# Kernel tuning notes

Measured on AMD Instinct MI355X. Metric: run time of the kernel, lower is better.

The kernel has to match this reference:

```python
import jax, jax.numpy as jnp
import numpy as np

N_NODES = 100000

def _sage_conv(x, src, dst, W_l, b_l, W_r):
    # PyG SAGEConv (aggr='mean'): out = lin_l(mean_{j in N(i)} x_j) + lin_r(x_i)
    msg = x[src]                                             # [E, d] gather
    agg = jax.ops.segment_sum(msg, dst, num_segments=N_NODES)  # [N, d]
    deg = jax.ops.segment_sum(jnp.ones((src.shape[0],), x.dtype), dst,
                              num_segments=N_NODES)          # [N]
    mean = agg / jnp.maximum(deg, 1.0)[:, None]
    return mean @ W_l + b_l + x @ W_r

def setup_inputs() -> dict:
    key = jax.random.key(0)
    ks = jax.random.split(key, 8)
    d_in, d_hid, d_out = 128, 128, 64
    E = 1_600_000
    x = jax.random.normal(ks[0], (N_NODES, d_in), dtype=jnp.float32)
    edge_index = jax.random.randint(ks[1], (2, E), 0, N_NODES, dtype=jnp.int64)
    s1 = 1.0 / np.sqrt(d_in)
    s2 = 1.0 / np.sqrt(d_hid)
    return {
        "x": x,
        "W1_l": jax.random.uniform(ks[2], (d_in, d_hid), jnp.float32, -s1, s1),
        "b1":   jnp.zeros((d_hid,), jnp.float32),
        "W1_r": jax.random.uniform(ks[3], (d_in, d_hid), jnp.float32, -s1, s1),
        "W2_l": jax.random.uniform(ks[4], (d_hid, d_out), jnp.float32, -s2, s2),
        "b2":   jnp.zeros((d_out,), jnp.float32),
        "W2_r": jax.random.uniform(ks[5], (d_hid, d_out), jnp.float32, -s2, s2),
        "edge_index": edge_index,
    }

def reference(x, W1_l, b1, W1_r, W2_l, b2, W2_r, edge_index):
    src, dst = edge_index[0], edge_index[1]
    h = _sage_conv(x, src, dst, W1_l, b1, W1_r)
    h = jax.nn.relu(h)
    # dropout is identity in eval mode (p=0.5 train-only); omitted for determinism
    out = _sage_conv(h, src, dst, W2_l, b2, W2_r)
    return out
```

## Files before the change

### kernel.cpp

```cpp
#include <hip/hip_runtime.h>
#include <hip/hip_bf16.h>
#include <cstdint>


typedef __bf16 bf16x8 __attribute__((ext_vector_type(8)));
typedef float f32x4 __attribute__((ext_vector_type(4)));
typedef float f32x2 __attribute__((ext_vector_type(2)));

#define MAXBUCK 800
#define CAP 2560
#define MAXEPT 16
#define P2B 512
#define HSTRIDE 136

__device__ __forceinline__ unsigned short f2bf(float f) {
    union { float f; unsigned int u; } v; v.f = f;
    unsigned int u = v.u;
    unsigned int r = ((u >> 16) & 1u) + 0x7fffu;
    return (unsigned short)((u + r) >> 16);
}

__device__ __forceinline__ f32x2 up2(unsigned int u) {
    uint2 t; t.x = u << 16; t.y = u & 0xffff0000u;
    return __builtin_bit_cast(f32x2, t);
}
__device__ __forceinline__ void accp(const uint4& v, f32x2* a) {
    a[0] += up2(v.x);
    a[1] += up2(v.y);
    a[2] += up2(v.z);
    a[3] += up2(v.w);
}
__device__ __forceinline__ void accpw(const uint4& v, float w, f32x2* a) {
    a[0] += up2(v.x) * w;
    a[1] += up2(v.y) * w;
    a[2] += up2(v.z) * w;
    a[3] += up2(v.w) * w;
}

__device__ __forceinline__ int edge_val(const int* ei32, const long long* ei64,
                                        int is64, size_t idx) {
    return is64 ? (int)ei64[idx] : ei32[idx];
}

__global__ __launch_bounds__(256) void fused_front(const float* __restrict__ x,
                                                   unsigned short* __restrict__ xb,
                                                   long long n8, int ncvt,
                                                   const float* __restrict__ W1l,
                                                   const float* __restrict__ W1r,
                                                   uint4* __restrict__ w1frag,
                                                   const float* __restrict__ W2l,
                                                   const float* __restrict__ W2r,
                                                   uint4* __restrict__ w2frag,
                                                   const int* __restrict__ ei32,
                                                   const long long* __restrict__ ei64,
                                                   int E, int ept, int nbuck,
                                                   int n_nodes,
                                                   int* __restrict__ bucket_pos,
                                                   unsigned* __restrict__ ebuf) {
    __shared__ int lhist[MAXBUCK];
    __shared__ int gbase[MAXBUCK];
    int b = blockIdx.x;
    if (b < P2B) {
        for (int i = threadIdx.x; i < nbuck; i += 256) lhist[i] = 0;
        __syncthreads();
        int is64;
        {
            int ok = 1;
            for (int i = 0; i < 8; ++i) {
                long long v = ei64[i];
                if (v < 0 || v >= n_nodes) ok = 0;
            }
            is64 = ok;
        }
        int base_e = b * (ept * 256);
        unsigned ed[MAXEPT];
        int bidx[MAXEPT];
        int slot[MAXEPT];
#pragma unroll 4
        for (int i = 0; i < ept; ++i) {
            int e = base_e + i * 256 + threadIdx.x;
            if (e < E) {
                int s = edge_val(ei32, ei64, is64, (size_t)e);
                int d = edge_val(ei32, ei64, is64, (size_t)E + e);
                ed[i] = ((unsigned)s << 7) | (unsigned)(d & 127);
                bidx[i] = d >> 7;
                slot[i] = atomicAdd(&lhist[d >> 7], 1);
            } else {
                slot[i] = -1;
            }
        }
        __syncthreads();
        for (int i = threadIdx.x; i < nbuck; i += 256) {
            int c = lhist[i];
            gbase[i] = c ? atomicAdd(&bucket_pos[i], c) : 0;
        }
        __syncthreads();
#pragma unroll 4
        for (int i = 0; i < ept; ++i) {
            if (slot[i] >= 0) {
                int pos = gbase[bidx[i]] + slot[i];
                if (pos < CAP) ebuf[(size_t)bidx[i] * CAP + pos] = ed[i];
            }
        }
        return;
    }
    int cb = b - P2B;
    if (cb < ncvt) {
        long long i = (long long)cb * 256 + threadIdx.x;
        if (i >= n8) return;
        const float4* p = (const float4*)(x + i * 8);
        float4 a = p[0], c = p[1];
        uint4 o;
        o.x = (unsigned)f2bf(a.x) | ((unsigned)f2bf(a.y) << 16);
        o.y = (unsigned)f2bf(a.z) | ((unsigned)f2bf(a.w) << 16);
        o.z = (unsigned)f2bf(c.x) | ((unsigned)f2bf(c.y) << 16);
        o.w = (unsigned)f2bf(c.z) | ((unsigned)f2bf(c.w) << 16);
        ((uint4*)(xb))[i] = o;
        return;
    }
    if (cb < ncvt + 16) {
        int tid = (cb - ncvt) * 256 + threadIdx.x;
        int fi = tid >> 6, lane = tid & 63;
        int ct = fi >> 3, ks = fi & 7;
        int k0 = ks * 32 + (lane >> 4) * 8;
        int n = ct * 16 + (lane & 15);
        unsigned short e[8];
#pragma unroll
        for (int j = 0; j < 8; ++j) {
            int k = k0 + j;
            float v = (k < 128) ? W1l[k * 128 + n] : W1r[(k - 128) * 128 + n];
            e[j] = f2bf(v);
        }
        uint4 o;
        o.x = (unsigned)e[0] | ((unsigned)e[1] << 16);
        o.y = (unsigned)e[2] | ((unsigned)e[3] << 16);
        o.z = (unsigned)e[4] | ((unsigned)e[5] << 16);
        o.w = (unsigned)e[6] | ((unsigned)e[7] << 16);
        w1frag[tid] = o;
        return;
    }
    int tid = (cb - ncvt - 16) * 256 + threadIdx.x;
    if (tid >= 2048) return;
    int fi = tid >> 6, lane = tid & 63;
    int ct = fi >> 2, ks = fi & 3;
    int k0 = ks * 32 + (lane >> 4) * 8;
    int n = ct * 16 + (lane & 15);
    unsigned short e[8];
#pragma unroll
    for (int j = 0; j < 8; ++j) {
        int k = k0 + j;
        float v = (n < 64) ? W2l[k * 64 + n] : W2r[k * 64 + (n - 64)];
        e[j] = f2bf(v);
    }
    uint4 o;
    o.x = (unsigned)e[0] | ((unsigned)e[1] << 16);
    o.y = (unsigned)e[2] | ((unsigned)e[3] << 16);
    o.z = (unsigned)e[4] | ((unsigned)e[5] << 16);
    o.w = (unsigned)e[6] | ((unsigned)e[7] << 16);
    w2frag[tid] = o;
}

__global__ __launch_bounds__(256) void pass3_finalize(const unsigned* __restrict__ ebuf,
                                                      const int* __restrict__ bucket_pos,
                                                      int nbuck, int N,
                                                      int2* __restrict__ startcnt,
                                                      int* __restrict__ csr) {
    __shared__ int lcnt[128];
    __shared__ int lexcl[128];
    __shared__ int sc[128];
    int b = blockIdx.x;
    int t = threadIdx.x;
    int d0 = b << 7;
    int nb = N - d0; if (nb > 128) nb = 128;
    int m = bucket_pos[b]; if (m > CAP) m = CAP;
    const unsigned* eb = ebuf + (size_t)b * CAP;

    if (t < 128) lcnt[t] = 0;
    __syncthreads();
    for (int j = t; j < m; j += 256) {
        atomicAdd(&lcnt[eb[j] & 127u], 1);
    }
    __syncthreads();
    int v = 0;
    if (t < 128) { v = lcnt[t]; sc[t] = v; }
    __syncthreads();
    for (int o = 1; o < 128; o <<= 1) {
        int x = 0;
        if (t < 128 && t >= o) x = sc[t - o];
        __syncthreads();
        if (t < 128 && t >= o) sc[t] += x;
        __syncthreads();
    }
    if (t < 128) {
        int excl = sc[t] - v;
        lexcl[t] = excl;
        if (t < nb) startcnt[d0 + t] = make_int2(b * CAP + excl, v);
        lcnt[t] = 0;
    }
    __syncthreads();
    for (int j = t; j < m; j += 256) {
        unsigned ed = eb[j];
        int li = (int)(ed & 127u);
        int slot = atomicAdd(&lcnt[li], 1);
        csr[b * CAP + lexcl[li] + slot] = (int)(ed >> 7);
    }
}

__global__ __launch_bounds__(256) void agg_mean128_bf(const unsigned short* __restrict__ Xb,
                                                      const int2* __restrict__ startcnt,
                                                      const int* __restrict__ csr,
                                                      unsigned short* __restrict__ outb,
                                                      int n_nodes) {
    int node = blockIdx.x * 4 + (threadIdx.x >> 6);
    if (node >= n_nodes) return;
    int lane = threadIdx.x & 63;
    int quad = lane >> 4;
    int l16 = lane & 15;
    int2 sc2 = startcnt[node];
    int s0 = sc2.x, deg = sc2.y, s1 = s0 + deg;
    f32x2 A0[4], A1[4];
#pragma unroll
    for (int k = 0; k < 4; ++k) { A0[k] = (f32x2){0.f, 0.f}; A1[k] = (f32x2){0.f, 0.f}; }
    int j = s0;
    for (; j + 8 <= s1; j += 8) {
        int p0 = csr[j + quad];
        int p1 = csr[j + 4 + quad];
        uint4 v0 = ((const uint4*)(Xb + (size_t)p0 * 128))[l16];
        uint4 v1 = ((const uint4*)(Xb + (size_t)p1 * 128))[l16];
        accp(v0, A0);
        accp(v1, A1);
    }
    if (j + 4 <= s1) {
        int p = csr[j + quad];
        uint4 v = ((const uint4*)(Xb + (size_t)p * 128))[l16];
        accp(v, A0);
        j += 4;
    }
    if (j < s1) {
        int jj = j + quad;
        int p = csr[(jj < s1) ? jj : (s1 - 1)];
        float w = (jj < s1) ? 1.0f : 0.0f;
        uint4 v = ((const uint4*)(Xb + (size_t)p * 128))[l16];
        accpw(v, w, A1);
    }
    float r[8];
#pragma unroll
    for (int k = 0; k < 4; ++k) {
        f32x2 s = A0[k] + A1[k];
        r[2 * k] = s.x;
        r[2 * k + 1] = s.y;
    }
#pragma unroll
    for (int k = 0; k < 8; ++k) r[k] += __shfl(r[k], lane ^ 16);
#pragma unroll
    for (int k = 0; k < 8; ++k) r[k] += __shfl(r[k], lane ^ 32);
    float inv = (deg > 0) ? 1.0f / (float)deg : 0.0f;
    if (quad == 0) {
        uint4 o;
        o.x = (unsigned)f2bf(r[0] * inv) | ((unsigned)f2bf(r[1] * inv) << 16);
        o.y = (unsigned)f2bf(r[2] * inv) | ((unsigned)f2bf(r[3] * inv) << 16);
        o.z = (unsigned)f2bf(r[4] * inv) | ((unsigned)f2bf(r[5] * inv) << 16);
        o.w = (unsigned)f2bf(r[6] * inv) | ((unsigned)f2bf(r[7] * inv) << 16);
        ((uint4*)(outb + (size_t)node * 128))[l16] = o;
    }
}

__global__ __launch_bounds__(256) void agg_mean64_bf_ep(const unsigned short* __restrict__ Zb,
                                                        const float* __restrict__ Wadd,
                                                        const int2* __restrict__ startcnt,
                                                        const int* __restrict__ csr,
                                                        float* __restrict__ out,
                                                        int n_nodes) {
    int node = blockIdx.x * 4 + (threadIdx.x >> 6);
    if (node >= n_nodes) return;
    int lane = threadIdx.x & 63;
    int oct = lane >> 3;
    int l8 = lane & 7;
    int2 sc2 = startcnt[node];
    int s0 = sc2.x, deg = sc2.y, s1 = s0 + deg;
    f32x2 A0[4], A1[4];
#pragma unroll
    for (int k = 0; k < 4; ++k) { A0[k] = (f32x2){0.f, 0.f}; A1[k] = (f32x2){0.f, 0.f}; }
    int j = s0;
    for (; j + 16 <= s1; j += 16) {
        int p0 = csr[j + oct];
        int p1 = csr[j + 8 + oct];
        uint4 v0 = ((const uint4*)(Zb + (size_t)p0 * 64))[l8];
        uint4 v1 = ((const uint4*)(Zb + (size_t)p1 * 64))[l8];
        accp(v0, A0);
        accp(v1, A1);
    }
    if (j + 8 <= s1) {
        int p = csr[j + oct];
        uint4 v = ((const uint4*)(Zb + (size_t)p * 64))[l8];
        accp(v, A0);
        j += 8;
    }
    if (j < s1) {
        int jj = j + oct;
        int p = csr[(jj < s1) ? jj : (s1 - 1)];
        float w = (jj < s1) ? 1.0f : 0.0f;
        uint4 v = ((const uint4*)(Zb + (size_t)p * 64))[l8];
        accpw(v, w, A1);
    }
    float r[8];
#pragma unroll
    for (int k = 0; k < 4; ++k) {
        f32x2 s = A0[k] + A1[k];
        r[2 * k] = s.x;
        r[2 * k + 1] = s.y;
    }
#pragma unroll
    for (int k = 0; k < 8; ++k) r[k] += __shfl(r[k], lane ^ 8);
#pragma unroll
    for (int k = 0; k < 8; ++k) r[k] += __shfl(r[k], lane ^ 16);
#pragma unroll
    for (int k = 0; k < 8; ++k) r[k] += __shfl(r[k], lane ^ 32);
    float inv = (deg > 0) ? 1.0f / (float)deg : 0.0f;
    if (oct == 0) {
        const float4* wp = (const float4*)(Wadd + (size_t)node * 64 + l8 * 8);
        float4 w0 = wp[0], w1 = wp[1];
        float4 o0, o1;
        o0.x = r[0] * inv + w0.x; o0.y = r[1] * inv + w0.y;
        o0.z = r[2] * inv + w0.z; o0.w = r[3] * inv + w0.w;
        o1.x = r[4] * inv + w1.x; o1.y = r[5] * inv + w1.y;
        o1.z = r[6] * inv + w1.z; o1.w = r[7] * inv + w1.w;
        float4* op = (float4*)(out + (size_t)node * 64 + l8 * 8);
        op[0] = o0; op[1] = o1;
    }
}

__global__ __launch_bounds__(256, 3) void gemm12_mfma(const unsigned short* __restrict__ meanb,
                                                      const unsigned short* __restrict__ xb,
                                                      const uint4* __restrict__ w1frag,
                                                      const uint4* __restrict__ w2frag,
                                                      const float* __restrict__ b1,
                                                      const float* __restrict__ b2,
                                                      unsigned short* __restrict__ z2,
                                                      float* __restrict__ w2out,
                                                      int nrows) {
    __shared__ unsigned short hs[4][32 * HSTRIDE];
    const int wid = threadIdx.x >> 6, lane = threadIdx.x & 63;
    const int quad = lane >> 4, l16 = lane & 15;
    const int m0 = blockIdx.x * 128 + wid * 32;
    unsigned short* hsw = &hs[wid][0];
    const uint4* w1p = w1frag + lane;
    const uint4* w2p = w2frag + lane;

    bf16x8 af[2][8];
#pragma unroll
    for (int mt = 0; mt < 2; ++mt) {
        int row = m0 + mt * 16 + l16;
        int rowc = (row < nrows) ? row : (nrows - 1);
        const uint4* mrow = (const uint4*)(meanb + (size_t)rowc * 128);
        const uint4* xrow = (const uint4*)(xb + (size_t)rowc * 128);
#pragma unroll
        for (int ks = 0; ks < 4; ++ks) {
            af[mt][ks]     = __builtin_bit_cast(bf16x8, mrow[ks * 4 + quad]);
            af[mt][ks + 4] = __builtin_bit_cast(bf16x8, xrow[ks * 4 + quad]);
        }
    }

    uint4 wc[8], wn[8];
#pragma unroll
    for (int ks = 0; ks < 8; ++ks) wc[ks] = w1p[ks * 64];
#pragma unroll
    for (int ct = 0; ct < 8; ++ct) {
        if (ct < 7) {
#pragma unroll
            for (int ks = 0; ks < 8; ++ks) wn[ks] = w1p[((ct + 1) * 8 + ks) * 64];
        }
        f32x4 a0 = (f32x4){0.f, 0.f, 0.f, 0.f};
        f32x4 a1 = (f32x4){0.f, 0.f, 0.f, 0.f};
#pragma unroll
        for (int ks = 0; ks < 8; ++ks) {
            bf16x8 bf = __builtin_bit_cast(bf16x8, wc[ks]);
            a0 = __builtin_amdgcn_mfma_f32_16x16x32_bf16(af[0][ks], bf, a0, 0, 0, 0);
            a1 = __builtin_amdgcn_mfma_f32_16x16x32_bf16(af[1][ks], bf, a1, 0, 0, 0);
        }
        int col = ct * 16 + l16;
        float bb = b1[col];
#pragma unroll
        for (int r = 0; r < 4; ++r) {
            hsw[(quad * 4 + r) * HSTRIDE + col] = f2bf(fmaxf(a0[r] + bb, 0.f));
            hsw[(16 + quad * 4 + r) * HSTRIDE + col] = f2bf(fmaxf(a1[r] + bb, 0.f));
        }
#pragma unroll
        for (int ks = 0; ks < 8; ++ks) wc[ks] = wn[ks];
    }

    bf16x8 af2[2][4];
#pragma unroll
    for (int mt = 0; mt < 2; ++mt)
#pragma unroll
        for (int ks = 0; ks < 4; ++ks) {
            uint4 t = *(const uint4*)(hsw + (mt * 16 + l16) * HSTRIDE + ks * 32 + quad * 8);
            af2[mt][ks] = __builtin_bit_cast(bf16x8, t);
        }

    uint4 wc2[4], wn2[4];
#pragma unroll
    for (int ks = 0; ks < 4; ++ks) wc2[ks] = w2p[ks * 64];
#pragma unroll
    for (int ct = 0; ct < 8; ++ct) {
        if (ct < 7) {
#pragma unroll
            for (int ks = 0; ks < 4; ++ks) wn2[ks] = w2p[((ct + 1) * 4 + ks) * 64];
        }
        f32x4 a0 = (f32x4){0.f, 0.f, 0.f, 0.f};
        f32x4 a1 = (f32x4){0.f, 0.f, 0.f, 0.f};
#pragma unroll
        for (int ks = 0; ks < 4; ++ks) {
            bf16x8 bf = __builtin_bit_cast(bf16x8, wc2[ks]);
            a0 = __builtin_amdgcn_mfma_f32_16x16x32_bf16(af2[0][ks], bf, a0, 0, 0, 0);
            a1 = __builtin_amdgcn_mfma_f32_16x16x32_bf16(af2[1][ks], bf, a1, 0, 0, 0);
        }
        int col = ct * 16 + l16;
#pragma unroll
        for (int mt = 0; mt < 2; ++mt) {
            f32x4 acc = mt ? a1 : a0;
#pragma unroll
            for (int r = 0; r < 4; ++r) {
                int orow = m0 + mt * 16 + quad * 4 + r;
                if (orow < nrows) {
                    if (col < 64) {
                        z2[(size_t)orow * 64 + col] = f2bf(acc[r]);
                    } else {
                        w2out[(size_t)orow * 64 + (col - 64)] = acc[r] + b2[col - 64];
                    }
                }
            }
        }
#pragma unroll
        for (int ks = 0; ks < 4; ++ks) wc2[ks] = wn2[ks];
    }
}

extern "C" void kernel_launch(void* const* d_in, const int* in_sizes, int n_in,
                              void* d_out, int out_size, void* d_ws, size_t ws_size,
                              hipStream_t stream) {
    const float* x    = (const float*)d_in[0];
    const float* W1_l = (const float*)d_in[1];
    const float* b1   = (const float*)d_in[2];
    const float* W1_r = (const float*)d_in[3];
    const float* W2_l = (const float*)d_in[4];
    const float* b2   = (const float*)d_in[5];
    const float* W2_r = (const float*)d_in[6];
    const void*  ei   = d_in[7];
    float* out = (float*)d_out;

    const int N = in_sizes[0] / 128;
    const int E = in_sizes[7] / 2;
    const int nbuck = (N + 127) >> 7;

    uintptr_t base = (uintptr_t)d_ws;
    int* bucket_pos = (int*)(base + 64);
    int2* startcnt = (int2*)(base + 8192);
    int* csr = (int*)((uintptr_t)(startcnt + N) + 255 & ~(uintptr_t)255);
    uintptr_t p = ((uintptr_t)(csr + (size_t)nbuck * CAP) + 255) & ~(uintptr_t)255;
    unsigned short* xb    = (unsigned short*)p; p += (size_t)N * 128 * 2;
    unsigned short* meanb = (unsigned short*)p; p += (size_t)N * 128 * 2;
    unsigned short* hbr   = (unsigned short*)p; p += (size_t)N * 128 * 2;
    uint4* w1frag = (uint4*)p; p += 4096 * 16;
    uint4* w2frag = (uint4*)p; p += 2048 * 16;
    unsigned* ebuf = (unsigned*)meanb;
    unsigned short* z2 = hbr;
    float* w2 = (float*)xb;

    const int* ei32 = (const int*)ei;
    const long long* ei64 = (const long long*)ei;

    hipMemsetAsync(bucket_pos, 0, (size_t)nbuck * sizeof(int), stream);

    long long n8 = (long long)N * 128 / 8;
    int ncvt = (int)((n8 + 255) / 256);
    int ept = (E + P2B * 256 - 1) / (P2B * 256);

    fused_front<<<P2B + ncvt + 24, 256, 0, stream>>>(
        x, xb, n8, ncvt, W1_l, W1_r, w1frag, W2_l, W2_r, w2frag,
        ei32, ei64, E, ept, nbuck, N, bucket_pos, ebuf);

    pass3_finalize<<<nbuck, 256, 0, stream>>>(ebuf, bucket_pos, nbuck, N,
                                              startcnt, csr);

    int ablocks = (N + 3) / 4;
    int gblocks = (N + 127) / 128;

    agg_mean128_bf<<<ablocks, 256, 0, stream>>>(xb, startcnt, csr, meanb, N);
    gemm12_mfma<<<gblocks, 256, 0, stream>>>(meanb, xb, w1frag, w2frag, b1, b2,
                                             z2, w2, N);
    agg_mean64_bf_ep<<<ablocks, 256, 0, stream>>>(z2, w2, startcnt, csr, out, N);
}
```

Baseline: 272.0 us.

## Fuse CSR finalize, layer-1 mean aggregation and both GEMMs into one kernel

Merges the bucket finalize, 128-wide mean aggregation and the fused layer-1/layer-2 MFMA GEMM into a single per-bucket kernel. The CSR slice is kept in LDS and the aggregated means are written straight into the per-wave LDS tile the GEMM reads, so the meanb round trip through global memory and two launches go away. In exchange, each 256-thread block now handles 128 nodes serially (32 per wave), so only about 782 blocks run, parallelism for the gather phase drops sharply, and LDS use per block grows. The workspace layout is also reorganised because ebuf and xb can no longer alias.

```diff
diff --git a/kernel.cpp b/kernel.cpp
--- a/kernel.cpp
+++ b/kernel.cpp
@@ -160,17 +160,27 @@
     w2frag[tid] = o;
 }
 
-__global__ __launch_bounds__(256) void pass3_finalize(const unsigned* __restrict__ ebuf,
-                                                      const int* __restrict__ bucket_pos,
-                                                      int nbuck, int N,
-                                                      int2* __restrict__ startcnt,
-                                                      int* __restrict__ csr) {
+__global__ __launch_bounds__(256, 3) void fused_mid(const unsigned* __restrict__ ebuf,
+                                                    const int* __restrict__ bucket_pos,
+                                                    const unsigned short* __restrict__ xb,
+                                                    const uint4* __restrict__ w1frag,
+                                                    const uint4* __restrict__ w2frag,
+                                                    const float* __restrict__ b1,
+                                                    const float* __restrict__ b2,
+                                                    int2* __restrict__ startcnt,
+                                                    int* __restrict__ csr,
+                                                    unsigned short* __restrict__ z2,
+                                                    float* __restrict__ w2out,
+                                                    int N) {
     __shared__ int lcnt[128];
     __shared__ int lexcl[128];
     __shared__ int sc[128];
-    int b = blockIdx.x;
-    int t = threadIdx.x;
-    int d0 = b << 7;
+    __shared__ int csr_s[CAP];
+    __shared__ unsigned short hs[4][32 * HSTRIDE];
+
+    const int b = blockIdx.x;
+    const int t = threadIdx.x;
+    const int d0 = b << 7;
     int nb = N - d0; if (nb > 128) nb = 128;
     int m = bucket_pos[b]; if (m > CAP) m = CAP;
     const unsigned* eb = ebuf + (size_t)b * CAP;
@@ -185,10 +195,10 @@
     if (t < 128) { v = lcnt[t]; sc[t] = v; }
     __syncthreads();
     for (int o = 1; o < 128; o <<= 1) {
-        int x = 0;
-        if (t < 128 && t >= o) x = sc[t - o];
+        int xx = 0;
+        if (t < 128 && t >= o) xx = sc[t - o];
         __syncthreads();
-        if (t < 128 && t >= o) sc[t] += x;
+        if (t < 128 && t >= o) sc[t] += xx;
         __syncthreads();
     }
     if (t < 128) {
@@ -202,66 +212,158 @@
         unsigned ed = eb[j];
         int li = (int)(ed & 127u);
         int slot = atomicAdd(&lcnt[li], 1);
-        csr[b * CAP + lexcl[li] + slot] = (int)(ed >> 7);
-    }
-}
-
-__global__ __launch_bounds__(256) void agg_mean128_bf(const unsigned short* __restrict__ Xb,
-                                                      const int2* __restrict__ startcnt,
-                                                      const int* __restrict__ csr,
-                                                      unsigned short* __restrict__ outb,
-                                                      int n_nodes) {
-    int node = blockIdx.x * 4 + (threadIdx.x >> 6);
-    if (node >= n_nodes) return;
-    int lane = threadIdx.x & 63;
-    int quad = lane >> 4;
-    int l16 = lane & 15;
-    int2 sc2 = startcnt[node];
-    int s0 = sc2.x, deg = sc2.y, s1 = s0 + deg;
-    f32x2 A0[4], A1[4];
-#pragma unroll
-    for (int k = 0; k < 4; ++k) { A0[k] = (f32x2){0.f, 0.f}; A1[k] = (f32x2){0.f, 0.f}; }
-    int j = s0;
-    for (; j + 8 <= s1; j += 8) {
-        int p0 = csr[j + quad];
-        int p1 = csr[j + 4 + quad];
-        uint4 v0 = ((const uint4*)(Xb + (size_t)p0 * 128))[l16];
-        uint4 v1 = ((const uint4*)(Xb + (size_t)p1 * 128))[l16];
-        accp(v0, A0);
-        accp(v1, A1);
-    }
-    if (j + 4 <= s1) {
-        int p = csr[j + quad];
-        uint4 v = ((const uint4*)(Xb + (size_t)p * 128))[l16];
-        accp(v, A0);
-        j += 4;
-    }
-    if (j < s1) {
-        int jj = j + quad;
-        int p = csr[(jj < s1) ? jj : (s1 - 1)];
-        float w = (jj < s1) ? 1.0f : 0.0f;
-        uint4 v = ((const uint4*)(Xb + (size_t)p * 128))[l16];
-        accpw(v, w, A1);
-    }
-    float r[8];
-#pragma unroll
-    for (int k = 0; k < 4; ++k) {
-        f32x2 s = A0[k] + A1[k];
-        r[2 * k] = s.x;
-        r[2 * k + 1] = s.y;
-    }
-#pragma unroll
-    for (int k = 0; k < 8; ++k) r[k] += __shfl(r[k], lane ^ 16);
-#pragma unroll
-    for (int k = 0; k < 8; ++k) r[k] += __shfl(r[k], lane ^ 32);
-    float inv = (deg > 0) ? 1.0f / (float)deg : 0.0f;
-    if (quad == 0) {
-        uint4 o;
-        o.x = (unsigned)f2bf(r[0] * inv) | ((unsigned)f2bf(r[1] * inv) << 16);
-        o.y = (unsigned)f2bf(r[2] * inv) | ((unsigned)f2bf(r[3] * inv) << 16);
-        o.z = (unsigned)f2bf(r[4] * inv) | ((unsigned)f2bf(r[5] * inv) << 16);
-        o.w = (unsigned)f2bf(r[6] * inv) | ((unsigned)f2bf(r[7] * inv) << 16);
-        ((uint4*)(outb + (size_t)node * 128))[l16] = o;
+        int pos = lexcl[li] + slot;
+        int sv = (int)(ed >> 7);
+        csr_s[pos] = sv;
+        csr[b * CAP + pos] = sv;
+    }
+    __syncthreads();
+
+    const int wid = t >> 6, lane = t & 63;
+    const int quad = lane >> 4, l16 = lane & 15;
+    unsigned short* hsw = &hs[wid][0];
+    for (int ln = 0; ln < 32; ++ln) {
+        int li = wid * 32 + ln;
+        int deg = lcnt[li];
+        int s0l = lexcl[li];
+        f32x2 A0[4], A1[4];
+#pragma unroll
+        for (int k = 0; k < 4; ++k) { A0[k] = (f32x2){0.f, 0.f}; A1[k] = (f32x2){0.f, 0.f}; }
+        int j = 0;
+        for (; j + 8 <= deg; j += 8) {
+            int p0 = csr_s[s0l + j + quad];
+            int p1 = csr_s[s0l + j + 4 + quad];
+            uint4 v0 = ((const uint4*)(xb + (size_t)p0 * 128))[l16];
+            uint4 v1 = ((const uint4*)(xb + (size_t)p1 * 128))[l16];
+            accp(v0, A0);
+            accp(v1, A1);
+        }
+        if (j + 4 <= deg) {
+            int p = csr_s[s0l + j + quad];
+            uint4 v0 = ((const uint4*)(xb + (size_t)p * 128))[l16];
+            accp(v0, A0);
+            j += 4;
+        }
+        if (j < deg) {
+            int jj = j + quad;
+            int p = csr_s[s0l + ((jj < deg) ? jj : (deg - 1))];
+            float w = (jj < deg) ? 1.0f : 0.0f;
+            uint4 v0 = ((const uint4*)(xb + (size_t)p * 128))[l16];
+            accpw(v0, w, A1);
+        }
+        float r[8];
+#pragma unroll
+        for (int k = 0; k < 4; ++k) {
+            f32x2 s = A0[k] + A1[k];
+            r[2 * k] = s.x;
+            r[2 * k + 1] = s.y;
+        }
+#pragma unroll
+        for (int k = 0; k < 8; ++k) r[k] += __shfl(r[k], lane ^ 16);
+#pragma unroll
+        for (int k = 0; k < 8; ++k) r[k] += __shfl(r[k], lane ^ 32);
+        float inv = (deg > 0) ? 1.0f / (float)deg : 0.0f;
+        if (quad == 0) {
+            uint4 o;
+            o.x = (unsigned)f2bf(r[0] * inv) | ((unsigned)f2bf(r[1] * inv) << 16);
+            o.y = (unsigned)f2bf(r[2] * inv) | ((unsigned)f2bf(r[3] * inv) << 16);
+            o.z = (unsigned)f2bf(r[4] * inv) | ((unsigned)f2bf(r[5] * inv) << 16);
+            o.w = (unsigned)f2bf(r[6] * inv) | ((unsigned)f2bf(r[7] * inv) << 16);
+            *(uint4*)(hsw + ln * HSTRIDE + l16 * 8) = o;
+        }
+    }
+
+    const int m0 = d0 + wid * 32;
+    const uint4* w1p = w1frag + lane;
+    const uint4* w2p = w2frag + lane;
+
+    bf16x8 af[2][8];
+#pragma unroll
+    for (int mt = 0; mt < 2; ++mt) {
+        int rl = mt * 16 + l16;
+        int grow = m0 + rl;
+        int rowc = (grow < N) ? grow : (N - 1);
+        const uint4* xrow = (const uint4*)(xb + (size_t)rowc * 128);
+#pragma unroll
+        for (int ks = 0; ks < 4; ++ks) {
+            af[mt][ks]     = __builtin_bit_cast(bf16x8,
+                *(const uint4*)(hsw + rl * HSTRIDE + ks * 32 + quad * 8));
+            af[mt][ks + 4] = __builtin_bit_cast(bf16x8, xrow[ks * 4 + quad]);
+        }
+    }
+
+    uint4 wc[8], wn[8];
+#pragma unroll
+    for (int ks = 0; ks < 8; ++ks) wc[ks] = w1p[ks * 64];
+#pragma unroll
+    for (int ct = 0; ct < 8; ++ct) {
+        if (ct < 7) {
+#pragma unroll
+            for (int ks = 0; ks < 8; ++ks) wn[ks] = w1p[((ct + 1) * 8 + ks) * 64];
+        }
+        f32x4 a0 = (f32x4){0.f, 0.f, 0.f, 0.f};
+        f32x4 a1 = (f32x4){0.f, 0.f, 0.f, 0.f};
+#pragma unroll
+        for (int ks = 0; ks < 8; ++ks) {
+            bf16x8 bf = __builtin_bit_cast(bf16x8, wc[ks]);
+            a0 = __builtin_amdgcn_mfma_f32_16x16x32_bf16(af[0][ks], bf, a0, 0, 0, 0);
+            a1 = __builtin_amdgcn_mfma_f32_16x16x32_bf16(af[1][ks], bf, a1, 0, 0, 0);
+        }
+        int col = ct * 16 + l16;
+        float bb = b1[col];
+#pragma unroll
+        for (int r = 0; r < 4; ++r) {
+            hsw[(quad * 4 + r) * HSTRIDE + col] = f2bf(fmaxf(a0[r] + bb, 0.f));
+            hsw[(16 + quad * 4 + r) * HSTRIDE + col] = f2bf(fmaxf(a1[r] + bb, 0.f));
+        }
+#pragma unroll
+        for (int ks = 0; ks < 8; ++ks) wc[ks] = wn[ks];
+    }
+
+    bf16x8 af2[2][4];
+#pragma unroll
+    for (int mt = 0; mt < 2; ++mt)
+#pragma unroll
+        for (int ks = 0; ks < 4; ++ks) {
+            uint4 tt = *(const uint4*)(hsw + (mt * 16 + l16) * HSTRIDE + ks * 32 + quad * 8);
+            af2[mt][ks] = __builtin_bit_cast(bf16x8, tt);
+        }
+
+    uint4 wc2[4], wn2[4];
+#pragma unroll
+    for (int ks = 0; ks < 4; ++ks) wc2[ks] = w2p[ks * 64];
+#pragma unroll
+    for (int ct = 0; ct < 8; ++ct) {
+        if (ct < 7) {
+#pragma unroll
+            for (int ks = 0; ks < 4; ++ks) wn2[ks] = w2p[((ct + 1) * 4 + ks) * 64];
+        }
+        f32x4 a0 = (f32x4){0.f, 0.f, 0.f, 0.f};
+        f32x4 a1 = (f32x4){0.f, 0.f, 0.f, 0.f};
+#pragma unroll
+        for (int ks = 0; ks < 4; ++ks) {
+            bf16x8 bf = __builtin_bit_cast(bf16x8, wc2[ks]);
+            a0 = __builtin_amdgcn_mfma_f32_16x16x32_bf16(af2[0][ks], bf, a0, 0, 0, 0);
+            a1 = __builtin_amdgcn_mfma_f32_16x16x32_bf16(af2[1][ks], bf, a1, 0, 0, 0);
+        }
+        int col = ct * 16 + l16;
+#pragma unroll
+        for (int mt = 0; mt < 2; ++mt) {
+            f32x4 acc = mt ? a1 : a0;
+#pragma unroll
+            for (int r = 0; r < 4; ++r) {
+                int orow = m0 + mt * 16 + quad * 4 + r;
+                if (orow < N) {
+                    if (col < 64) {
+                        z2[(size_t)orow * 64 + col] = f2bf(acc[r]);
+                    } else {
+                        w2out[(size_t)orow * 64 + (col - 64)] = acc[r] + b2[col - 64];
+                    }
+                }
+            }
+        }
+#pragma unroll
+        for (int ks = 0; ks < 4; ++ks) wc2[ks] = wn2[ks];
     }
 }
 
@@ -330,112 +432,6 @@
     }
 }
 
-__global__ __launch_bounds__(256, 3) void gemm12_mfma(const unsigned short* __restrict__ meanb,
-                                                      const unsigned short* __restrict__ xb,
-                                                      const uint4* __restrict__ w1frag,
-                                                      const uint4* __restrict__ w2frag,
-                                                      const float* __restrict__ b1,
-                                                      const float* __restrict__ b2,
-                                                      unsigned short* __restrict__ z2,
-                                                      float* __restrict__ w2out,
-                                                      int nrows) {
-    __shared__ unsigned short hs[4][32 * HSTRIDE];
-    const int wid = threadIdx.x >> 6, lane = threadIdx.x & 63;
-    const int quad = lane >> 4, l16 = lane & 15;
-    const int m0 = blockIdx.x * 128 + wid * 32;
-    unsigned short* hsw = &hs[wid][0];
-    const uint4* w1p = w1frag + lane;
-    const uint4* w2p = w2frag + lane;
-
-    bf16x8 af[2][8];
-#pragma unroll
-    for (int mt = 0; mt < 2; ++mt) {
-        int row = m0 + mt * 16 + l16;
-        int rowc = (row < nrows) ? row : (nrows - 1);
-        const uint4* mrow = (const uint4*)(meanb + (size_t)rowc * 128);
-        const uint4* xrow = (const uint4*)(xb + (size_t)rowc * 128);
-#pragma unroll
-        for (int ks = 0; ks < 4; ++ks) {
-            af[mt][ks]     = __builtin_bit_cast(bf16x8, mrow[ks * 4 + quad]);
-            af[mt][ks + 4] = __builtin_bit_cast(bf16x8, xrow[ks * 4 + quad]);
-        }
-    }
-
-    uint4 wc[8], wn[8];
-#pragma unroll
-    for (int ks = 0; ks < 8; ++ks) wc[ks] = w1p[ks * 64];
-#pragma unroll
-    for (int ct = 0; ct < 8; ++ct) {
-        if (ct < 7) {
-#pragma unroll
-            for (int ks = 0; ks < 8; ++ks) wn[ks] = w1p[((ct + 1) * 8 + ks) * 64];
-        }
-        f32x4 a0 = (f32x4){0.f, 0.f, 0.f, 0.f};
-        f32x4 a1 = (f32x4){0.f, 0.f, 0.f, 0.f};
-#pragma unroll
-        for (int ks = 0; ks < 8; ++ks) {
-            bf16x8 bf = __builtin_bit_cast(bf16x8, wc[ks]);
-            a0 = __builtin_amdgcn_mfma_f32_16x16x32_bf16(af[0][ks], bf, a0, 0, 0, 0);
-            a1 = __builtin_amdgcn_mfma_f32_16x16x32_bf16(af[1][ks], bf, a1, 0, 0, 0);
-        }
-        int col = ct * 16 + l16;
-        float bb = b1[col];
-#pragma unroll
-        for (int r = 0; r < 4; ++r) {
-            hsw[(quad * 4 + r) * HSTRIDE + col] = f2bf(fmaxf(a0[r] + bb, 0.f));
-            hsw[(16 + quad * 4 + r) * HSTRIDE + col] = f2bf(fmaxf(a1[r] + bb, 0.f));
-        }
-#pragma unroll
-        for (int ks = 0; ks < 8; ++ks) wc[ks] = wn[ks];
-    }
-
-    bf16x8 af2[2][4];
-#pragma unroll
-    for (int mt = 0; mt < 2; ++mt)
-#pragma unroll
-        for (int ks = 0; ks < 4; ++ks) {
-            uint4 t = *(const uint4*)(hsw + (mt * 16 + l16) * HSTRIDE + ks * 32 + quad * 8);
-            af2[mt][ks] = __builtin_bit_cast(bf16x8, t);
-        }
-
-    uint4 wc2[4], wn2[4];
-#pragma unroll
-    for (int ks = 0; ks < 4; ++ks) wc2[ks] = w2p[ks * 64];
-#pragma unroll
-    for (int ct = 0; ct < 8; ++ct) {
-        if (ct < 7) {
-#pragma unroll
-            for (int ks = 0; ks < 4; ++ks) wn2[ks] = w2p[((ct + 1) * 4 + ks) * 64];
-        }
-        f32x4 a0 = (f32x4){0.f, 0.f, 0.f, 0.f};
-        f32x4 a1 = (f32x4){0.f, 0.f, 0.f, 0.f};
-#pragma unroll
-        for (int ks = 0; ks < 4; ++ks) {
-            bf16x8 bf = __builtin_bit_cast(bf16x8, wc2[ks]);
-            a0 = __builtin_amdgcn_mfma_f32_16x16x32_bf16(af2[0][ks], bf, a0, 0, 0, 0);
-            a1 = __builtin_amdgcn_mfma_f32_16x16x32_bf16(af2[1][ks], bf, a1, 0, 0, 0);
-        }
-        int col = ct * 16 + l16;
-#pragma unroll
-        for (int mt = 0; mt < 2; ++mt) {
-            f32x4 acc = mt ? a1 : a0;
-#pragma unroll
-            for (int r = 0; r < 4; ++r) {
-                int orow = m0 + mt * 16 + quad * 4 + r;
-                if (orow < nrows) {
-                    if (col < 64) {
-                        z2[(size_t)orow * 64 + col] = f2bf(acc[r]);
-                    } else {
-                        w2out[(size_t)orow * 64 + (col - 64)] = acc[r] + b2[col - 64];
-                    }
-                }
-            }
-        }
-#pragma unroll
-        for (int ks = 0; ks < 4; ++ks) wc2[ks] = wn2[ks];
-    }
-}
-
 extern "C" void kernel_launch(void* const* d_in, const int* in_sizes, int n_in,
                               void* d_out, int out_size, void* d_ws, size_t ws_size,
                               hipStream_t stream) {
@@ -456,16 +452,15 @@
     uintptr_t base = (uintptr_t)d_ws;
     int* bucket_pos = (int*)(base + 64);
     int2* startcnt = (int2*)(base + 8192);
-    int* csr = (int*)((uintptr_t)(startcnt + N) + 255 & ~(uintptr_t)255);
-    uintptr_t p = ((uintptr_t)(csr + (size_t)nbuck * CAP) + 255) & ~(uintptr_t)255;
-    unsigned short* xb    = (unsigned short*)p; p += (size_t)N * 128 * 2;
-    unsigned short* meanb = (unsigned short*)p; p += (size_t)N * 128 * 2;
-    unsigned short* hbr   = (unsigned short*)p; p += (size_t)N * 128 * 2;
-    uint4* w1frag = (uint4*)p; p += 4096 * 16;
-    uint4* w2frag = (uint4*)p; p += 2048 * 16;
-    unsigned* ebuf = (unsigned*)meanb;
-    unsigned short* z2 = hbr;
-    float* w2 = (float*)xb;
+    uintptr_t p = ((uintptr_t)(startcnt + N) + 255) & ~(uintptr_t)255;
+    int* csr = (int*)p;                p += (size_t)nbuck * CAP * 4;
+    p = (p + 255) & ~(uintptr_t)255;
+    unsigned short* xb = (unsigned short*)p; p += (size_t)N * 128 * 2;
+    unsigned* ebuf = (unsigned*)p;     p += (size_t)nbuck * CAP * 4;
+    unsigned short* z2 = (unsigned short*)p; p += (size_t)N * 64 * 2;
+    float* w2 = (float*)p;             p += (size_t)N * 64 * 4;
+    uint4* w1frag = (uint4*)p;         p += 4096 * 16;
+    uint4* w2frag = (uint4*)p;         p += 2048 * 16;
 
     const int* ei32 = (const int*)ei;
     const long long* ei64 = (const long long*)ei;
@@ -480,14 +475,9 @@
         x, xb, n8, ncvt, W1_l, W1_r, w1frag, W2_l, W2_r, w2frag,
         ei32, ei64, E, ept, nbuck, N, bucket_pos, ebuf);
 
-    pass3_finalize<<<nbuck, 256, 0, stream>>>(ebuf, bucket_pos, nbuck, N,
-                                              startcnt, csr);
+    fused_mid<<<nbuck, 256, 0, stream>>>(ebuf, bucket_pos, xb, w1frag, w2frag,
+                                         b1, b2, startcnt, csr, z2, w2, N);
 
     int ablocks = (N + 3) / 4;
-    int gblocks = (N + 127) / 128;
-
-    agg_mean128_bf<<<ablocks, 256, 0, stream>>>(xb, startcnt, csr, meanb, N);
-    gemm12_mfma<<<gblocks, 256, 0, stream>>>(meanb, xb, w1frag, w2frag, b1, b2,
-                                             z2, w2, N);
     agg_mean64_bf_ep<<<ablocks, 256, 0, stream>>>(z2, w2, startcnt, csr, out, N);
 }
```

Result: slower. 303.4 us (+11.5%).

## Stage bucketed edges in LDS so global scatter writes are contiguous per bucket

Applied to the files above, without the earlier changes.

The edge-bucketing phase now computes a block-local exclusive scan of the bucket histogram. Each edge is placed into shared-memory staging arrays sorted by bucket, then written out to the global edge buffer with consecutive threads hitting consecutive positions within each bucket. Before, every thread scattered its edges straight to random global locations. The goal is better write coalescing for the scatter. In exchange it adds about 24KB of shared memory, which can lower occupancy for all block types in the fused kernel, plus a scan and extra barriers.

```diff
diff --git a/kernel.cpp b/kernel.cpp
--- a/kernel.cpp
+++ b/kernel.cpp
@@ -11,6 +11,7 @@
 #define CAP 2560
 #define MAXEPT 16
 #define P2B 512
+#define P2E (MAXEPT * 256)
 #define HSTRIDE 136
 
 __device__ __forceinline__ unsigned short f2bf(float f) {
@@ -58,10 +59,15 @@
                                                    int* __restrict__ bucket_pos,
                                                    unsigned* __restrict__ ebuf) {
     __shared__ int lhist[MAXBUCK];
+    __shared__ int lexcl[MAXBUCK];
     __shared__ int gbase[MAXBUCK];
+    __shared__ int part[256];
+    __shared__ unsigned estage[P2E];
+    __shared__ unsigned short bstage[P2E];
     int b = blockIdx.x;
+    int t = threadIdx.x;
     if (b < P2B) {
-        for (int i = threadIdx.x; i < nbuck; i += 256) lhist[i] = 0;
+        for (int i = t; i < nbuck; i += 256) lhist[i] = 0;
         __syncthreads();
         int is64;
         {
@@ -78,7 +84,7 @@
         int slot[MAXEPT];
 #pragma unroll 4
         for (int i = 0; i < ept; ++i) {
-            int e = base_e + i * 256 + threadIdx.x;
+            int e = base_e + i * 256 + t;
             if (e < E) {
                 int s = edge_val(ei32, ei64, is64, (size_t)e);
                 int d = edge_val(ei32, ei64, is64, (size_t)E + e);
@@ -90,7 +96,29 @@
             }
         }
         __syncthreads();
-        for (int i = threadIdx.x; i < nbuck; i += 256) {
+        int base4 = t * 4;
+        int c0 = (base4 + 0 < nbuck) ? lhist[base4 + 0] : 0;
+        int c1 = (base4 + 1 < nbuck) ? lhist[base4 + 1] : 0;
+        int c2 = (base4 + 2 < nbuck) ? lhist[base4 + 2] : 0;
+        int c3 = (base4 + 3 < nbuck) ? lhist[base4 + 3] : 0;
+        int lsum = c0 + c1 + c2 + c3;
+        part[t] = lsum;
+        __syncthreads();
+        for (int o = 1; o < 256; o <<= 1) {
+            int xv = 0;
+            if (t >= o) xv = part[t - o];
+            __syncthreads();
+            if (t >= o) part[t] += xv;
+            __syncthreads();
+        }
+        {
+            int run = part[t] - lsum;
+            if (base4 + 0 < nbuck) { lexcl[base4 + 0] = run; run += c0; }
+            if (base4 + 1 < nbuck) { lexcl[base4 + 1] = run; run += c1; }
+            if (base4 + 2 < nbuck) { lexcl[base4 + 2] = run; run += c2; }
+            if (base4 + 3 < nbuck) { lexcl[base4 + 3] = run; run += c3; }
+        }
+        for (int i = t; i < nbuck; i += 256) {
             int c = lhist[i];
             gbase[i] = c ? atomicAdd(&bucket_pos[i], c) : 0;
         }
@@ -98,15 +126,25 @@
 #pragma unroll 4
         for (int i = 0; i < ept; ++i) {
             if (slot[i] >= 0) {
-                int pos = gbase[bidx[i]] + slot[i];
-                if (pos < CAP) ebuf[(size_t)bidx[i] * CAP + pos] = ed[i];
+                int pos = lexcl[bidx[i]] + slot[i];
+                estage[pos] = ed[i];
+                bstage[pos] = (unsigned short)bidx[i];
             }
+        }
+        __syncthreads();
+        int m_blk = E - base_e;
+        if (m_blk < 0) m_blk = 0;
+        if (m_blk > ept * 256) m_blk = ept * 256;
+        for (int s = t; s < m_blk; s += 256) {
+            int bb = bstage[s];
+            int pos = gbase[bb] + (s - lexcl[bb]);
+            if (pos < CAP) ebuf[(size_t)bb * CAP + pos] = estage[s];
         }
         return;
     }
     int cb = b - P2B;
     if (cb < ncvt) {
-        long long i = (long long)cb * 256 + threadIdx.x;
+        long long i = (long long)cb * 256 + t;
         if (i >= n8) return;
         const float4* p = (const float4*)(x + i * 8);
         float4 a = p[0], c = p[1];
@@ -119,7 +157,7 @@
         return;
     }
     if (cb < ncvt + 16) {
-        int tid = (cb - ncvt) * 256 + threadIdx.x;
+        int tid = (cb - ncvt) * 256 + t;
         int fi = tid >> 6, lane = tid & 63;
         int ct = fi >> 3, ks = fi & 7;
         int k0 = ks * 32 + (lane >> 4) * 8;
@@ -139,7 +177,7 @@
         w1frag[tid] = o;
         return;
     }
-    int tid = (cb - ncvt - 16) * 256 + threadIdx.x;
+    int tid = (cb - ncvt - 16) * 256 + t;
     if (tid >= 2048) return;
     int fi = tid >> 6, lane = tid & 63;
     int ct = fi >> 2, ks = fi & 3;
```

New measurement: 270.8 us. About the same (-0.5%).
